# Optimization experiments

Measured on AMD Instinct MI355X. Metric: run time of the kernel, lower is better.

## Reference

```python
import jax, jax.numpy as jnp
import numpy as np

WS = 8  # window_size
EPS = 1e-5  # BatchNorm eps


def setup_inputs() -> dict:
    key = jax.random.key(0)
    ks = jax.random.split(key, 11)
    c = 64
    return {
        "x": jax.random.normal(ks[0], (4, c, 256, 256), dtype=jnp.float32),
        "w_in": jax.random.normal(ks[1], (c, c), dtype=jnp.float32) * 0.05,
        "b_in": jax.random.normal(ks[2], (c,), dtype=jnp.float32) * 0.05,
        "bn_gamma": jax.random.uniform(ks[3], (c,), dtype=jnp.float32),
        "bn_beta": jax.random.normal(ks[4], (c,), dtype=jnp.float32) * 0.05,
        "bn_mean": jax.random.normal(ks[5], (c,), dtype=jnp.float32) * 0.05,
        "bn_var": jax.random.uniform(ks[6], (c,), dtype=jnp.float32),
        "w_mask": jax.random.normal(ks[7], (c, c), dtype=jnp.float32) * 0.05,
        "b_mask": jax.random.normal(ks[8], (c,), dtype=jnp.float32) * 0.05,
        "w_out": jax.random.normal(ks[9], (c, c), dtype=jnp.float32) * 0.05,
        "b_out": jax.random.normal(ks[10], (c,), dtype=jnp.float32) * 0.05,
    }


def reference(x, w_in, b_in, bn_gamma, bn_beta, bn_mean, bn_var,
              w_mask, b_mask, w_out, b_out):
    ws = WS
    b, c, h, w = x.shape  # shifts == 0 -> no roll

    # project_inp: 1x1 conv + BatchNorm2d (inference mode, running stats)
    x = jnp.einsum('bchw,oc->bohw', x, w_in) + b_in[None, :, None, None]
    inv = bn_gamma / jnp.sqrt(bn_var + EPS)
    x = (x - bn_mean[None, :, None, None]) * inv[None, :, None, None] \
        + bn_beta[None, :, None, None]

    # seq_refl_win_pad(back=False): pad right/bottom by ws, then copy the
    # preceding ws rows into the bottom pad, then the preceding ws cols
    # (including the new bottom rows) into the right pad.
    x_pad = jnp.concatenate([x, x[:, :, -ws:, :]], axis=2)      # [b,c,h+ws,w]
    x_pad = jnp.concatenate([x_pad, x_pad[:, :, :, -ws:]], axis=3)  # [b,c,h+ws,w+ws]

    hh, ww = h // ws, w // ws
    # mask = Conv2d(kernel=1, stride=2) on the 2ws x 2ws windows ->
    # equivalent to sampling even offsets inside each window, then a 1x1 linear.
    row = (jnp.arange(hh) * ws)[:, None] + jnp.arange(0, 2 * ws, 2)[None, :]  # [hh, ws]
    col = (jnp.arange(ww) * ws)[:, None] + jnp.arange(0, 2 * ws, 2)[None, :]  # [ww, ws]
    g = x_pad[:, :, row, :]        # [b, c, hh, ws_h, w+ws]
    g = g[:, :, :, :, col]         # [b, c, hh, ws_h, ww, ws_w]
    # torch's double unfold yields window dims ordered (W-window, H-window),
    # and q flattens in that (Wwin, Hwin) order -> match exactly.
    g = jnp.transpose(g, (0, 2, 4, 5, 3, 1))        # [b, hh, ww, ws_w, ws_h, c]
    q = g.reshape(b * hh * ww, ws * ws, c)
    q = q @ w_mask.T + b_mask                       # 1x1 conv as per-pixel linear

    # v: non-overlapping ws x ws windows of x, flattened H-major (dh dw)
    v = x.reshape(b, c, hh, ws, ww, ws)
    v = jnp.transpose(v, (0, 2, 4, 3, 5, 1)).reshape(b * hh * ww, ws * ws, c)

    atn = jax.nn.softmax(q @ jnp.swapaxes(q, -1, -2), axis=-1)  # [bn, ws^2, ws^2]
    y = atn @ v                                                  # [bn, ws^2, c]

    # reassemble: '(b h w) (dh dw) c -> b c (h dh) (w dw)'
    y = y.reshape(b, hh, ww, ws, ws, c)
    y = jnp.transpose(y, (0, 5, 1, 3, 2, 4)).reshape(b, c, h, w)

    # project_out: 1x1 conv
    y = jnp.einsum('bchw,oc->bohw', y, w_out) + b_out[None, :, None, None]
    return y
```

## Files before the change

kernel.cpp:

```cpp
#include <hip/hip_runtime.h>

typedef unsigned short ushort_t;
typedef unsigned int uint_t;
typedef __attribute__((ext_vector_type(8))) short short8v;
typedef __attribute__((ext_vector_type(4))) float f32x4;

__device__ __forceinline__ float bf2f(ushort_t u) {
    union { uint_t u; float f; } v; v.u = (uint_t)u << 16; return v.f;
}
__device__ __forceinline__ ushort_t f2bf(float f) {
    union { float f; uint_t u; } v; v.f = f;
    uint_t u = v.u;
    return (ushort_t)((u + 0x7fffu + ((u >> 16) & 1u)) >> 16);
}

__global__ __launch_bounds__(256) void k1_pwbn(
    const float* __restrict__ x, const float* __restrict__ w_in, const float* __restrict__ b_in,
    const float* __restrict__ gamma, const float* __restrict__ beta,
    const float* __restrict__ mean, const float* __restrict__ var,
    ushort_t* __restrict__ xbn)
{
    __shared__ float Xt[64][132];
    __shared__ float WT[64][68];
    __shared__ float bef[64];

    int tid = threadIdx.x;
    int b   = blockIdx.x >> 9;
    int hw0 = (blockIdx.x & 511) << 7;
    const float* xb = x + ((size_t)b << 22);

    for (int e = 0; e < 16; ++e) {
        int idx = e * 256 + tid;
        int o = idx >> 6, c = idx & 63;
        WT[c][o] = w_in[idx] * gamma[o] * rsqrtf(var[o] + 1e-5f);
    }
    if (tid < 64) {
        float inv = gamma[tid] * rsqrtf(var[tid] + 1e-5f);
        bef[tid] = (b_in[tid] - mean[tid]) * inv + beta[tid];
    }
    for (int e = 0; e < 8; ++e) {
        int i16 = e * 256 + tid;
        int c = i16 >> 5, s = i16 & 31;
        *(float4*)&Xt[c][s * 4] = *(const float4*)(xb + ((size_t)c << 16) + hw0 + s * 4);
    }
    __syncthreads();

    int tr = tid >> 3, tc = tid & 7;
    float acc[4][8];
    #pragma unroll
    for (int p = 0; p < 4; ++p)
        #pragma unroll
        for (int q = 0; q < 8; ++q) acc[p][q] = 0.f;

    for (int c = 0; c < 64; ++c) {
        float4 a4 = *(const float4*)&Xt[c][4 * tr];
        float4 b0 = *(const float4*)&WT[c][8 * tc];
        float4 b1 = *(const float4*)&WT[c][8 * tc + 4];
        float av[4] = {a4.x, a4.y, a4.z, a4.w};
        float bv[8] = {b0.x, b0.y, b0.z, b0.w, b1.x, b1.y, b1.z, b1.w};
        #pragma unroll
        for (int p = 0; p < 4; ++p)
            #pragma unroll
            for (int q = 0; q < 8; ++q) acc[p][q] += av[p] * bv[q];
    }

    float bo[8];
    #pragma unroll
    for (int q = 0; q < 8; ++q) bo[q] = bef[8 * tc + q];
    ushort_t* xp = xbn + ((size_t)(b * 65536 + hw0 + 4 * tr) << 6) + 8 * tc;
    #pragma unroll
    for (int p = 0; p < 4; ++p) {
        union { int4 v; ushort_t s[8]; } pk;
        #pragma unroll
        for (int q = 0; q < 8; ++q) pk.s[q] = f2bf(acc[p][q] + bo[q]);
        *(int4*)(xp + (size_t)p * 64) = pk.v;
    }
}

#define LDS_G    0
#define LDS_V    9216
#define LDS_WMH  18432
#define LDS_WML  27648
#define LDS_QH   36864
#define LDS_QL   46080
#define LDS_WOH  55296
#define LDS_WOL  64512
#define LDS_RED  73728
#define LDS_RED2 74752
#define LDS_RS   75776
#define LDS_TOT  76032

#define MFMA(A,B,C) __builtin_amdgcn_mfma_f32_16x16x32_bf16(A, B, C, 0, 0, 0)

__device__ __forceinline__ void splitw(const float* src, short* dh, short* dl) {
    union { int4 v; ushort_t s[8]; } h0, h1, l0, l1;
    float4 f0 = *(const float4*)(src);
    float4 f1 = *(const float4*)(src + 4);
    float4 f2 = *(const float4*)(src + 8);
    float4 f3 = *(const float4*)(src + 12);
    float fv[16] = {f0.x,f0.y,f0.z,f0.w, f1.x,f1.y,f1.z,f1.w,
                    f2.x,f2.y,f2.z,f2.w, f3.x,f3.y,f3.z,f3.w};
    #pragma unroll
    for (int e = 0; e < 8; ++e) {
        ushort_t h = f2bf(fv[e]);     h0.s[e] = h; l0.s[e] = f2bf(fv[e] - bf2f(h));
        ushort_t g = f2bf(fv[e + 8]); h1.s[e] = g; l1.s[e] = f2bf(fv[e + 8] - bf2f(g));
    }
    *(int4*)(dh)     = h0.v;
    *(int4*)(dh + 8) = h1.v;
    *(int4*)(dl)     = l0.v;
    *(int4*)(dl + 8) = l1.v;
}

__global__ __launch_bounds__(256, 2) void k2_attn_mfma(
    const ushort_t* __restrict__ xbn,
    const float* __restrict__ w_mask, const float* __restrict__ b_mask,
    const float* __restrict__ w_out,  const float* __restrict__ b_out,
    float* __restrict__ out)
{
    __shared__ char smem[LDS_TOT];
    short* gb   = (short*)(smem + LDS_G);
    short* vb   = (short*)(smem + LDS_V);
    short* wmh  = (short*)(smem + LDS_WMH);
    short* wml  = (short*)(smem + LDS_WML);
    short* qhb  = (short*)(smem + LDS_QH);
    short* qlb  = (short*)(smem + LDS_QL);
    short* woh  = (short*)(smem + LDS_WOH);
    short* wol  = (short*)(smem + LDS_WOL);
    float* Sb   = (float*)(smem + LDS_WMH);
    short* vwt  = (short*)(smem + LDS_G);
    short* pt   = (short*)(smem + LDS_V);
    float* outt = (float*)(smem + LDS_WMH);
    float* red  = (float*)(smem + LDS_RED);
    float* red2 = (float*)(smem + LDS_RED2);
    float* rsv  = (float*)(smem + LDS_RS);

    int tid = threadIdx.x;
    int wid = blockIdx.x;
    int b = wid >> 10, i = (wid >> 5) & 31, j = wid & 31;
    const ushort_t* xb = xbn + ((size_t)b << 22);

    {
        int t = tid >> 2, seg = tid & 3;
        int r = t & 7, s = t >> 3;
        int pr = i * 8 + 2 * r; if (pr >= 256) pr -= 8;
        int pc = j * 8 + 2 * s; if (pc >= 256) pc -= 8;
        const ushort_t* src = xb + (((size_t)((pr << 8) | pc)) << 6) + seg * 16;
        *(int4*)(gb + t * 72 + seg * 16)     = *(const int4*)src;
        *(int4*)(gb + t * 72 + seg * 16 + 8) = *(const int4*)(src + 8);
        int vr = i * 8 + (t >> 3), vc = j * 8 + (t & 7);
        const ushort_t* vsrc = xb + (((size_t)((vr << 8) | vc)) << 6) + seg * 16;
        *(int4*)(vb + t * 72 + seg * 16)     = *(const int4*)vsrc;
        *(int4*)(vb + t * 72 + seg * 16 + 8) = *(const int4*)(vsrc + 8);
        splitw(w_mask + t * 64 + seg * 16, wmh + t * 72 + seg * 16, wml + t * 72 + seg * 16);
    }
    __syncthreads();

    int w = tid >> 6, l = tid & 63;
    int half = l >> 4, lr = l & 15;
    int mrow = (16 * w + lr) * 72;
    int kc0 = half * 8, kc1 = 32 + half * 8;

    {
        int t = tid >> 2, seg = tid & 3;
        splitw(w_out + t * 64 + seg * 16, woh + t * 72 + seg * 16, wol + t * 72 + seg * 16);
    }

    {
        short8v amh0 = *(short8v*)(wmh + mrow + kc0);
        short8v amh1 = *(short8v*)(wmh + mrow + kc1);
        short8v aml0 = *(short8v*)(wml + mrow + kc0);
        short8v aml1 = *(short8v*)(wml + mrow + kc1);
        float4 bm = *(const float4*)(b_mask + 16 * w + half * 4);
        float bmv[4] = {bm.x, bm.y, bm.z, bm.w};
        #pragma unroll
        for (int n = 0; n < 4; ++n) {
            int nrow = (16 * n + lr) * 72;
            short8v bg0 = *(short8v*)(gb + nrow + kc0);
            short8v bg1 = *(short8v*)(gb + nrow + kc1);
            f32x4 acc = {0.f, 0.f, 0.f, 0.f};
            acc = MFMA(amh0, bg0, acc);
            acc = MFMA(amh1, bg1, acc);
            acc = MFMA(aml0, bg0, acc);
            acc = MFMA(aml1, bg1, acc);
            ushort_t hs[4], ls[4];
            #pragma unroll
            for (int rr = 0; rr < 4; ++rr) {
                float qv = acc[rr] + bmv[rr];
                hs[rr] = f2bf(qv);
                ls[rr] = f2bf(qv - bf2f(hs[rr]));
            }
            int qoff = (16 * n + lr) * 72 + 16 * w + half * 4;
            *(uint2*)(qhb + qoff) = make_uint2((uint_t)hs[0] | ((uint_t)hs[1] << 16),
                                               (uint_t)hs[2] | ((uint_t)hs[3] << 16));
            *(uint2*)(qlb + qoff) = make_uint2((uint_t)ls[0] | ((uint_t)ls[1] << 16),
                                               (uint_t)ls[2] | ((uint_t)ls[3] << 16));
        }
    }
    __syncthreads();

    {
        short8v av0 = *(short8v*)(vb + mrow + kc0);
        short8v av1 = *(short8v*)(vb + mrow + kc1);
        #pragma unroll
        for (int n = 0; n < 4; ++n) {
            int nrow = (16 * n + lr) * 72;
            short8v bh0 = *(short8v*)(woh + nrow + kc0);
            short8v bh1 = *(short8v*)(woh + nrow + kc1);
            short8v bl0 = *(short8v*)(wol + nrow + kc0);
            short8v bl1 = *(short8v*)(wol + nrow + kc1);
            f32x4 acc = {0.f, 0.f, 0.f, 0.f};
            acc = MFMA(av0, bh0, acc);
            acc = MFMA(av1, bh1, acc);
            acc = MFMA(av0, bl0, acc);
            acc = MFMA(av1, bl1, acc);
            ushort_t hs[4];
            #pragma unroll
            for (int rr = 0; rr < 4; ++rr) hs[rr] = f2bf(acc[rr]);
            int voff = (16 * n + lr) * 72 + 16 * w + half * 4;
            *(uint2*)(vwt + voff) = make_uint2((uint_t)hs[0] | ((uint_t)hs[1] << 16),
                                               (uint_t)hs[2] | ((uint_t)hs[3] << 16));
        }
    }
    {
        short8v ah0 = *(short8v*)(qhb + mrow + kc0);
        short8v ah1 = *(short8v*)(qhb + mrow + kc1);
        short8v al0 = *(short8v*)(qlb + mrow + kc0);
        short8v al1 = *(short8v*)(qlb + mrow + kc1);
        #pragma unroll
        for (int n = 0; n < 4; ++n) {
            int nrow = (16 * n + lr) * 72;
            short8v bh0 = *(short8v*)(qhb + nrow + kc0);
            short8v bh1 = *(short8v*)(qhb + nrow + kc1);
            short8v bl0 = *(short8v*)(qlb + nrow + kc0);
            short8v bl1 = *(short8v*)(qlb + nrow + kc1);
            f32x4 acc = {0.f, 0.f, 0.f, 0.f};
            acc = MFMA(ah0, bh0, acc);
            acc = MFMA(ah1, bh1, acc);
            acc = MFMA(ah0, bl0, acc);
            acc = MFMA(ah1, bl1, acc);
            acc = MFMA(al0, bh0, acc);
            acc = MFMA(al1, bh1, acc);
            *(f32x4*)(Sb + (16 * n + lr) * 68 + 16 * w + half * 4) = acc;
        }
    }
    __syncthreads();

    {
        int row = tid >> 2, p = tid & 3;
        const float* srow = Sb + row * 68 + p * 16;
        float4 s4[4];
        #pragma unroll
        for (int q = 0; q < 4; ++q) s4[q] = *(const float4*)(srow + 4 * q);
        float m = -1e30f;
        #pragma unroll
        for (int q = 0; q < 4; ++q)
            m = fmaxf(m, fmaxf(fmaxf(s4[q].x, s4[q].y), fmaxf(s4[q].z, s4[q].w)));
        red[row * 4 + p] = m;
        __syncthreads();
        m = fmaxf(fmaxf(red[row * 4 + 0], red[row * 4 + 1]),
                  fmaxf(red[row * 4 + 2], red[row * 4 + 3]));
        union { int4 v; ushort_t s[8]; } pk0, pk1;
        float ssum = 0.f;
        #pragma unroll
        for (int q = 0; q < 4; ++q) {
            float vv[4] = {s4[q].x, s4[q].y, s4[q].z, s4[q].w};
            #pragma unroll
            for (int e = 0; e < 4; ++e) {
                ushort_t h = f2bf(__expf(vv[e] - m));
                ssum += bf2f(h);
                if (q < 2) pk0.s[q * 4 + e] = h; else pk1.s[(q - 2) * 4 + e] = h;
            }
        }
        *(int4*)(pt + row * 72 + p * 16)     = pk0.v;
        *(int4*)(pt + row * 72 + p * 16 + 8) = pk1.v;
        red2[row * 4 + p] = ssum;
        __syncthreads();
        if (p == 0)
            rsv[row] = 1.0f / (red2[row * 4] + red2[row * 4 + 1] +
                               red2[row * 4 + 2] + red2[row * 4 + 3]);
    }
    __syncthreads();

    {
        short8v ap0 = *(short8v*)(pt + mrow + kc0);
        short8v ap1 = *(short8v*)(pt + mrow + kc1);
        float4 rv = *(const float4*)(rsv + 16 * w + half * 4);
        float rvv[4] = {rv.x, rv.y, rv.z, rv.w};
        f32x4 oacc[4];
        #pragma unroll
        for (int n = 0; n < 4; ++n) {
            int nrow = (16 * n + lr) * 72;
            short8v bv0 = *(short8v*)(vwt + nrow + kc0);
            short8v bv1 = *(short8v*)(vwt + nrow + kc1);
            f32x4 acc = {0.f, 0.f, 0.f, 0.f};
            acc = MFMA(ap0, bv0, acc);
            acc = MFMA(ap1, bv1, acc);
            oacc[n] = acc;
        }
        __syncthreads();
        #pragma unroll
        for (int n = 0; n < 4; ++n) {
            float bo = b_out[16 * n + lr];
            float4 wv = make_float4(oacc[n][0] * rvv[0] + bo, oacc[n][1] * rvv[1] + bo,
                                    oacc[n][2] * rvv[2] + bo, oacc[n][3] * rvv[3] + bo);
            *(float4*)(outt + (16 * n + lr) * 68 + 16 * w + half * 4) = wv;
        }
    }
    __syncthreads();

    {
        float* ob = out + ((size_t)b << 22);
        int base = (i * 8) * 256 + j * 8;
        for (int pp = 0; pp < 16; ++pp) {
            int e = pp * 256 + tid;
            int o = e >> 6, t = e & 63;
            ob[((size_t)o << 16) + base + ((t >> 3) << 8) + (t & 7)] = outt[o * 68 + t];
        }
    }
}

extern "C" void kernel_launch(void* const* d_in, const int* in_sizes, int n_in,
                              void* d_out, int out_size, void* d_ws, size_t ws_size,
                              hipStream_t stream) {
    const float* x      = (const float*)d_in[0];
    const float* w_in   = (const float*)d_in[1];
    const float* b_in   = (const float*)d_in[2];
    const float* gamma  = (const float*)d_in[3];
    const float* beta   = (const float*)d_in[4];
    const float* mean   = (const float*)d_in[5];
    const float* var    = (const float*)d_in[6];
    const float* w_mask = (const float*)d_in[7];
    const float* b_mask = (const float*)d_in[8];
    const float* w_out  = (const float*)d_in[9];
    const float* b_out  = (const float*)d_in[10];
    float* out = (float*)d_out;
    ushort_t* xbn = (ushort_t*)d_ws;

    hipLaunchKernelGGL(k1_pwbn, dim3(2048), dim3(256), 0, stream,
                       x, w_in, b_in, gamma, beta, mean, var, xbn);
    hipLaunchKernelGGL(k2_attn_mfma, dim3(4096), dim3(256), 0, stream,
                       xbn, w_mask, b_mask, w_out, b_out, out);
}
```

Measured before the change: 201.5 us.

## Rewrite input projection kernel with split-bf16 MFMA instead of FP32 FMAs

The pointwise conv + BatchNorm kernel now splits x and the BN-folded weights into bf16 high/low parts in LDS and computes the 64x64 channel mix with three bf16 MFMAs per k-chunk, replacing the scalar FP32 outer-product loop. Tiles shrink to 64 pixels per block, so twice as many blocks are launched, and occupancy is hinted at 4 blocks per CU. The aim is to offload the arithmetic to matrix cores and leave the kernel limited by memory bandwidth. The three-term split keeps accuracy close to FP32, at the cost of the conversion work and a smaller tile per block.

```diff
diff --git a/kernel.cpp b/kernel.cpp
--- a/kernel.cpp
+++ b/kernel.cpp
@@ -14,66 +14,104 @@
     return (ushort_t)((u + 0x7fffu + ((u >> 16) & 1u)) >> 16);
 }
 
-__global__ __launch_bounds__(256) void k1_pwbn(
+#define MFMA(A,B,C) __builtin_amdgcn_mfma_f32_16x16x32_bf16(A, B, C, 0, 0, 0)
+
+__global__ __launch_bounds__(256, 4) void k1_pwbn_mfma(
     const float* __restrict__ x, const float* __restrict__ w_in, const float* __restrict__ b_in,
     const float* __restrict__ gamma, const float* __restrict__ beta,
     const float* __restrict__ mean, const float* __restrict__ var,
     ushort_t* __restrict__ xbn)
 {
-    __shared__ float Xt[64][132];
-    __shared__ float WT[64][68];
+    __shared__ short xsh[64][72];
+    __shared__ short xsl[64][72];
+    __shared__ short wfh[64][72];
+    __shared__ short wfl[64][72];
     __shared__ float bef[64];
 
     int tid = threadIdx.x;
-    int b   = blockIdx.x >> 9;
-    int hw0 = (blockIdx.x & 511) << 7;
+    int b   = blockIdx.x >> 10;
+    int hw0 = (blockIdx.x & 1023) << 6;
     const float* xb = x + ((size_t)b << 22);
 
-    for (int e = 0; e < 16; ++e) {
-        int idx = e * 256 + tid;
-        int o = idx >> 6, c = idx & 63;
-        WT[c][o] = w_in[idx] * gamma[o] * rsqrtf(var[o] + 1e-5f);
+    #pragma unroll
+    for (int u = 0; u < 2; ++u) {
+        int idx = u * 256 + tid;
+        int cp = idx >> 4, pq = idx & 15;
+        int c0 = cp * 2, p0 = pq * 4;
+        float4 fa = *(const float4*)(xb + (size_t)c0 * 65536 + hw0 + p0);
+        float4 fb = *(const float4*)(xb + (size_t)(c0 + 1) * 65536 + hw0 + p0);
+        float va[4] = {fa.x, fa.y, fa.z, fa.w};
+        float vb[4] = {fb.x, fb.y, fb.z, fb.w};
+        #pragma unroll
+        for (int e = 0; e < 4; ++e) {
+            ushort_t h0 = f2bf(va[e]), h1 = f2bf(vb[e]);
+            ushort_t l0 = f2bf(va[e] - bf2f(h0)), l1 = f2bf(vb[e] - bf2f(h1));
+            *(uint_t*)&xsh[p0 + e][c0] = (uint_t)h0 | ((uint_t)h1 << 16);
+            *(uint_t*)&xsl[p0 + e][c0] = (uint_t)l0 | ((uint_t)l1 << 16);
+        }
+    }
+    #pragma unroll
+    for (int v = 0; v < 2; ++v) {
+        int idx = v * 256 + tid;
+        int o = idx >> 3, c0 = (idx & 7) * 8;
+        float sc = gamma[o] * rsqrtf(var[o] + 1e-5f);
+        float4 fa = *(const float4*)(w_in + o * 64 + c0);
+        float4 fb = *(const float4*)(w_in + o * 64 + c0 + 4);
+        float vv[8] = {fa.x, fa.y, fa.z, fa.w, fb.x, fb.y, fb.z, fb.w};
+        union { int4 q; ushort_t s[8]; } ph, pl;
+        #pragma unroll
+        for (int e = 0; e < 8; ++e) {
+            float wv = vv[e] * sc;
+            ushort_t h = f2bf(wv);
+            ph.s[e] = h;
+            pl.s[e] = f2bf(wv - bf2f(h));
+        }
+        *(int4*)&wfh[o][c0] = ph.q;
+        *(int4*)&wfl[o][c0] = pl.q;
     }
     if (tid < 64) {
         float inv = gamma[tid] * rsqrtf(var[tid] + 1e-5f);
         bef[tid] = (b_in[tid] - mean[tid]) * inv + beta[tid];
     }
-    for (int e = 0; e < 8; ++e) {
-        int i16 = e * 256 + tid;
-        int c = i16 >> 5, s = i16 & 31;
-        *(float4*)&Xt[c][s * 4] = *(const float4*)(xb + ((size_t)c << 16) + hw0 + s * 4);
-    }
-    __syncthreads();
-
-    int tr = tid >> 3, tc = tid & 7;
-    float acc[4][8];
-    #pragma unroll
-    for (int p = 0; p < 4; ++p)
-        #pragma unroll
-        for (int q = 0; q < 8; ++q) acc[p][q] = 0.f;
-
-    for (int c = 0; c < 64; ++c) {
-        float4 a4 = *(const float4*)&Xt[c][4 * tr];
-        float4 b0 = *(const float4*)&WT[c][8 * tc];
-        float4 b1 = *(const float4*)&WT[c][8 * tc + 4];
-        float av[4] = {a4.x, a4.y, a4.z, a4.w};
-        float bv[8] = {b0.x, b0.y, b0.z, b0.w, b1.x, b1.y, b1.z, b1.w};
-        #pragma unroll
-        for (int p = 0; p < 4; ++p)
-            #pragma unroll
-            for (int q = 0; q < 8; ++q) acc[p][q] += av[p] * bv[q];
-    }
-
-    float bo[8];
-    #pragma unroll
-    for (int q = 0; q < 8; ++q) bo[q] = bef[8 * tc + q];
-    ushort_t* xp = xbn + ((size_t)(b * 65536 + hw0 + 4 * tr) << 6) + 8 * tc;
-    #pragma unroll
-    for (int p = 0; p < 4; ++p) {
-        union { int4 v; ushort_t s[8]; } pk;
-        #pragma unroll
-        for (int q = 0; q < 8; ++q) pk.s[q] = f2bf(acc[p][q] + bo[q]);
-        *(int4*)(xp + (size_t)p * 64) = pk.v;
+    __syncthreads();
+
+    int w = tid >> 6, l = tid & 63;
+    int half = l >> 4, lr = l & 15;
+    int k0 = half * 8;
+
+    short8v bh[2], bl[2];
+    #pragma unroll
+    for (int kc = 0; kc < 2; ++kc) {
+        bh[kc] = *(short8v*)&xsh[16 * w + lr][k0 + 32 * kc];
+        bl[kc] = *(short8v*)&xsl[16 * w + lr][k0 + 32 * kc];
+    }
+    short8v ah[4][2], al[4][2];
+    #pragma unroll
+    for (int ot = 0; ot < 4; ++ot)
+        #pragma unroll
+        for (int kc = 0; kc < 2; ++kc) {
+            ah[ot][kc] = *(short8v*)&wfh[16 * ot + lr][k0 + 32 * kc];
+            al[ot][kc] = *(short8v*)&wfl[16 * ot + lr][k0 + 32 * kc];
+        }
+
+    ushort_t* xp = xbn + ((size_t)(b * 65536 + hw0 + 16 * w + lr) << 6);
+    #pragma unroll
+    for (int ot = 0; ot < 4; ++ot) {
+        f32x4 acc = {0.f, 0.f, 0.f, 0.f};
+        #pragma unroll
+        for (int kc = 0; kc < 2; ++kc) {
+            acc = MFMA(ah[ot][kc], bh[kc], acc);
+            acc = MFMA(ah[ot][kc], bl[kc], acc);
+            acc = MFMA(al[ot][kc], bh[kc], acc);
+        }
+        int o0 = 16 * ot + 4 * half;
+        float4 bq = *(const float4*)&bef[o0];
+        float bqs[4] = {bq.x, bq.y, bq.z, bq.w};
+        ushort_t hs[4];
+        #pragma unroll
+        for (int rr = 0; rr < 4; ++rr) hs[rr] = f2bf(acc[rr] + bqs[rr]);
+        *(uint2*)(xp + o0) = make_uint2((uint_t)hs[0] | ((uint_t)hs[1] << 16),
+                                        (uint_t)hs[2] | ((uint_t)hs[3] << 16));
     }
 }
 
@@ -89,8 +127,6 @@
 #define LDS_RED2 74752
 #define LDS_RS   75776
 #define LDS_TOT  76032
-
-#define MFMA(A,B,C) __builtin_amdgcn_mfma_f32_16x16x32_bf16(A, B, C, 0, 0, 0)
 
 __device__ __forceinline__ void splitw(const float* src, short* dh, short* dl) {
     union { int4 v; ushort_t s[8]; } h0, h1, l0, l1;
@@ -336,7 +372,7 @@
     float* out = (float*)d_out;
     ushort_t* xbn = (ushort_t*)d_ws;
 
-    hipLaunchKernelGGL(k1_pwbn, dim3(2048), dim3(256), 0, stream,
+    hipLaunchKernelGGL(k1_pwbn_mfma, dim3(4096), dim3(256), 0, stream,
                        x, w_in, b_in, gamma, beta, mean, var, xbn);
     hipLaunchKernelGGL(k2_attn_mfma, dim3(4096), dim3(256), 0, stream,
                        xbn, w_mask, b_mask, w_out, b_out, out);
```

Result: faster. 194.7 us (-3.3%).
